# Kernel tuning notes

Measured on AMD Instinct MI355X. Metric: run time of the kernel, lower is better.

## Reference

```python
import jax, jax.numpy as jnp
import numpy as np

CONV_NUM = 8
CONV_SIZE = 96
HIDDEN = 768  # = CONV_NUM * CONV_SIZE
MAX_LEN = 128


def get_entity(x, s, e):
    # x: [B, L, H]; mean of x[i, s[i]:max(e[i], s[i]+1)] per sample (ragged gather+mean)
    e = jnp.maximum(e, s + 1)
    pos = jnp.arange(x.shape[1])  # [L]
    mask = (pos[None, :] >= s[:, None]) & (pos[None, :] < e[:, None])  # [B, L]
    m = mask.astype(x.dtype)
    return jnp.einsum('blh,bl->bh', x, m) / jnp.sum(m, axis=1, keepdims=True)


def feature_abstract(head_ent, tail_ent, x, fc_W, fc_b):
    # head_ent/tail_ent: [B, HIDDEN] -> per-sample conv filters; x: [B, HIDDEN]
    B = x.shape[0]
    wh = head_ent.reshape(B * CONV_NUM, 1, 1, CONV_SIZE)
    wt = tail_ent.reshape(B * CONV_NUM, 1, 1, CONV_SIZE)
    lhs = x.reshape(1, B, 1, HIDDEN)  # NCHW, groups=B -> per-sample correlation
    h = jax.nn.relu(jax.lax.conv_general_dilated(lhs, wh, (1, 1), 'VALID', feature_group_count=B))
    t = jax.nn.relu(jax.lax.conv_general_dilated(lhs, wt, (1, 1), 'VALID', feature_group_count=B))
    # h,t: [1, B*CONV_NUM, 1, T] with T = HIDDEN - CONV_SIZE + 1
    ht = jnp.concatenate([h, t], axis=3).reshape(B * CONV_NUM, -1)  # [B*cn, 2T]
    ht = ht.reshape(B * CONV_NUM, -1, 2).mean(axis=-1)  # AvgPool1d(k=2, s=2) -> [B*cn, T]
    flat = ht.reshape(B, -1)  # [B, cn*T] (dropout is identity in eval)
    return flat @ fc_W.T + fc_b  # [B, HIDDEN]


def setup_inputs() -> dict:
    key = jax.random.key(0)
    ks = jax.random.split(key, 16)
    Bs, Bq, L, H = 400, 1200, MAX_LEN, HIDDEN

    def spans(k1, k2, B):
        s = jax.random.randint(k1, (B,), 0, 100)
        e = jnp.minimum(s + jax.random.randint(k2, (B,), 1, 20), L)
        return s.astype(jnp.int64), e.astype(jnp.int64)

    s_eh, s_eh_end = spans(ks[0], ks[1], Bs)
    s_et, s_et_end = spans(ks[2], ks[3], Bs)
    q_eh, q_eh_end = spans(ks[4], ks[5], Bq)
    q_et, q_et_end = spans(ks[6], ks[7], Bq)
    fc_in = (H - CONV_SIZE + 1) * CONV_NUM  # 5384
    return {
        'all_support': jax.random.normal(ks[8], (Bs, L, H), jnp.float32),
        'support_emb': jax.random.normal(ks[9], (Bs, H), jnp.float32),
        'all_query': jax.random.normal(ks[10], (Bq, L, H), jnp.float32),
        'query_emb': jax.random.normal(ks[11], (Bq, H), jnp.float32),
        'fc_W': jax.random.normal(ks[12], (H, fc_in), jnp.float32) / np.sqrt(fc_in),
        'fc_b': jnp.zeros((H,), jnp.float32),
        's_eh': s_eh, 's_eh_end': s_eh_end, 's_et': s_et, 's_et_end': s_et_end,
        'q_eh': q_eh, 'q_eh_end': q_eh_end, 'q_et': q_et, 'q_et_end': q_et_end,
        'N': 10, 'K': 5, 'total_Q': 150,
    }


def reference(all_support, support_emb, all_query, query_emb, fc_W, fc_b,
              s_eh, s_eh_end, s_et, s_et_end, q_eh, q_eh_end, q_et, q_et_end,
              N, K, total_Q):
    sh = get_entity(all_support, s_eh, s_eh_end)
    st = get_entity(all_support, s_et, s_et_end)
    qh = get_entity(all_query, q_eh, q_eh_end)
    qt = get_entity(all_query, q_et, q_et_end)

    sup = feature_abstract(sh, st, support_emb, fc_W, fc_b).reshape(-1, N, K, HIDDEN)
    qry = feature_abstract(qh, qt, query_emb, fc_W, fc_b).reshape(-1, total_Q, HIDDEN)

    proto = sup.mean(axis=2)  # [Be, N, H]
    # -||proto - query||^2 over feature dim -> [Be, total_Q, N]
    diff = proto[:, None, :, :] - qry[:, :, None, :]
    logits = -jnp.sum(diff * diff, axis=-1)
    minn = logits.min(axis=-1)
    logits = jnp.concatenate([logits, minn[..., None] - 1.0], axis=2)  # [Be, total_Q, N+1]
    pred = jnp.argmax(logits.reshape(-1, N + 1), axis=1)
    return logits, pred
```

## Files before the change

kernel.cpp:

```cpp
#include <hip/hip_runtime.h>

#define H        768
#define LMAX     128
#define CONV_NUM 8
#define CONV_SIZE 96
#define T_CONV   673
#define FC_IN    5384
#define KP       5408
#define KSTEPS   (KP / 32)
#define N_WAY    10
#define K_SHOT   5
#define TOTAL_Q  150
#define SPLITK   8
#define BS       400
#define BQ       1200
#define MTOT     1600
#define NPROTO   80
#define MA       1280

using s16x8 = __attribute__((ext_vector_type(8))) short;
using f32x4 = __attribute__((ext_vector_type(4))) float;
typedef unsigned short u16;

__device__ __forceinline__ u16 f2bf(float x) {
    unsigned u = __float_as_uint(x);
    u += 0x7FFFu + ((u >> 16) & 1u);
    return (u16)(u >> 16);
}
__device__ __forceinline__ float bf2f(u16 b) { return __uint_as_float(((unsigned)b) << 16); }

__device__ __forceinline__ void gl16(const u16* g, u16* l) {
    __builtin_amdgcn_global_load_lds(
        (const __attribute__((address_space(1))) unsigned int*)g,
        (__attribute__((address_space(3))) unsigned int*)l, 16, 0, 0);
}

#define HTS 678
#define XCS 784
__global__ __launch_bounds__(256, 4) void pre_kernel(
    const float* __restrict__ all_support, const float* __restrict__ all_query,
    const float* __restrict__ support_emb, const float* __restrict__ query_emb,
    const float* __restrict__ fc_W,
    const int* __restrict__ s_eh, const int* __restrict__ s_eh_end,
    const int* __restrict__ s_et, const int* __restrict__ s_et_end,
    const int* __restrict__ q_eh, const int* __restrict__ q_eh_end,
    const int* __restrict__ q_et, const int* __restrict__ q_et_end,
    u16* __restrict__ flatS, u16* __restrict__ A_bf,
    u16* __restrict__ Wh)
{
    int bid = blockIdx.x;
    int tid = threadIdx.x;

    if (bid >= MTOT) {
        int r = bid - MTOT;
        const float* wr = fc_W + (size_t)r * FC_IN;
        u16* whr = Wh + (size_t)r * KP;
        for (int j4 = tid; j4 < KP / 4; j4 += 256) {
            int j = j4 * 4;
            ushort4 o;
            if (j4 < FC_IN / 4) {
                float4 v = *(const float4*)(wr + j);
                o.x = f2bf(v.x); o.y = f2bf(v.y); o.z = f2bf(v.z); o.w = f2bf(v.w);
            } else {
                o.x = 0; o.y = 0; o.z = 0; o.w = 0;
            }
            *(ushort4*)(whr + j) = o;
        }
        return;
    }

    __shared__ u16 htb[16 * HTS];
    __shared__ u16 filt_h[16 * 96];
    __shared__ u16 filt_l[16 * 96];
    __shared__ u16 xcs[8][XCS];

    int b = bid;
    const float* src;
    int sh, eh, st, et;
    if (b < BS) {
        src = all_support + (size_t)b * LMAX * H;
        sh = s_eh[b]; eh = s_eh_end[b]; st = s_et[b]; et = s_et_end[b];
    } else {
        int m = b - BS;
        src = all_query + (size_t)m * LMAX * H;
        sh = q_eh[m]; eh = q_eh_end[m]; st = q_et[m]; et = q_et_end[m];
    }
    if (eh < sh + 1) eh = sh + 1;
    if (et < st + 1) et = st + 1;

    {
        float a0 = 0.f, a1 = 0.f, a2 = 0.f, b0 = 0.f, b1 = 0.f, b2 = 0.f;
        float c0 = 0.f, c1 = 0.f, c2 = 0.f, d0 = 0.f, d1 = 0.f, d2 = 0.f;
        int r = sh;
        for (; r + 4 <= eh; r += 4) {
            const float* p0 = src + (size_t)r * H;
            const float* p1 = p0 + H;
            const float* p2 = p0 + 2 * H;
            const float* p3 = p0 + 3 * H;
            a0 += p0[tid]; a1 += p0[tid + 256]; a2 += p0[tid + 512];
            b0 += p1[tid]; b1 += p1[tid + 256]; b2 += p1[tid + 512];
            c0 += p2[tid]; c1 += p2[tid + 256]; c2 += p2[tid + 512];
            d0 += p3[tid]; d1 += p3[tid + 256]; d2 += p3[tid + 512];
        }
        for (; r < eh; ++r) {
            const float* p0 = src + (size_t)r * H;
            a0 += p0[tid]; a1 += p0[tid + 256]; a2 += p0[tid + 512];
        }
        float rc = 1.0f / (float)(eh - sh);
        float m0 = ((a0 + b0) + (c0 + d0)) * rc;
        float m1 = ((a1 + b1) + (c1 + d1)) * rc;
        float m2 = ((a2 + b2) + (c2 + d2)) * rc;
        u16 h0 = f2bf(m0), h1 = f2bf(m1), h2 = f2bf(m2);
        filt_h[tid] = h0;       filt_l[tid] = f2bf(m0 - bf2f(h0));
        filt_h[tid + 256] = h1; filt_l[tid + 256] = f2bf(m1 - bf2f(h1));
        filt_h[tid + 512] = h2; filt_l[tid + 512] = f2bf(m2 - bf2f(h2));
        a0 = a1 = a2 = b0 = b1 = b2 = c0 = c1 = c2 = d0 = d1 = d2 = 0.f;
        r = st;
        for (; r + 4 <= et; r += 4) {
            const float* p0 = src + (size_t)r * H;
            const float* p1 = p0 + H;
            const float* p2 = p0 + 2 * H;
            const float* p3 = p0 + 3 * H;
            a0 += p0[tid]; a1 += p0[tid + 256]; a2 += p0[tid + 512];
            b0 += p1[tid]; b1 += p1[tid + 256]; b2 += p1[tid + 512];
            c0 += p2[tid]; c1 += p2[tid + 256]; c2 += p2[tid + 512];
            d0 += p3[tid]; d1 += p3[tid + 256]; d2 += p3[tid + 512];
        }
        for (; r < et; ++r) {
            const float* p0 = src + (size_t)r * H;
            a0 += p0[tid]; a1 += p0[tid + 256]; a2 += p0[tid + 512];
        }
        rc = 1.0f / (float)(et - st);
        m0 = ((a0 + b0) + (c0 + d0)) * rc;
        m1 = ((a1 + b1) + (c1 + d1)) * rc;
        m2 = ((a2 + b2) + (c2 + d2)) * rc;
        h0 = f2bf(m0); h1 = f2bf(m1); h2 = f2bf(m2);
        filt_h[tid + 768] = h0;  filt_l[tid + 768] = f2bf(m0 - bf2f(h0));
        filt_h[tid + 1024] = h1; filt_l[tid + 1024] = f2bf(m1 - bf2f(h1));
        filt_h[tid + 1280] = h2; filt_l[tid + 1280] = f2bf(m2 - bf2f(h2));
    }

    {
        if (tid < 192) {
            int row = tid / 24, idx = tid % 24;
            int j = 768 - row + idx;
            if (j < XCS) xcs[row][j] = 0;
        }
        if (tid >= 192 && tid < 192 + 80) {
            int t = tid - 192;
            htb[(t / 5) * HTS + 673 + (t % 5)] = 0;
        }
        const float* xsrc = (b < BS) ? (support_emb + (size_t)b * H)
                                     : (query_emb + (size_t)(b - BS) * H);
        if (tid < 192) {
            float4 v = *(const float4*)(xsrc + tid * 4);
            u16 h[4] = {f2bf(v.x), f2bf(v.y), f2bf(v.z), f2bf(v.w)};
            #pragma unroll
            for (int u = 0; u < 4; ++u) {
                int i = tid * 4 + u;
                #pragma unroll
                for (int c = 0; c < 8; ++c)
                    if (i >= c) xcs[c][i - c] = h[u];
            }
        }
    }
    __syncthreads();

    {
        int lane = tid & 63, wv = tid >> 6;
        int n = lane & 15, g = lane >> 4;
        int afo = n * 96 + g * 8;
        s16x8 fh0 = *(const s16x8*)&filt_h[afo];
        s16x8 fh1 = *(const s16x8*)&filt_h[afo + 32];
        s16x8 fh2 = *(const s16x8*)&filt_h[afo + 64];
        s16x8 fl0 = *(const s16x8*)&filt_l[afo];
        s16x8 fl1 = *(const s16x8*)&filt_l[afo + 32];
        s16x8 fl2 = *(const s16x8*)&filt_l[afo + 64];
        const u16* xrow = &xcs[n & 7][g * 8 + (n & 8)];
        #pragma unroll 1
        for (int nt = wv; nt < 43; nt += 4) {
            const u16* xp = xrow + nt * 16;
            s16x8 x0 = *(const s16x8*)(xp);
            s16x8 x1 = *(const s16x8*)(xp + 32);
            s16x8 x2 = *(const s16x8*)(xp + 64);
            f32x4 a = (f32x4){0.f, 0.f, 0.f, 0.f};
            a = __builtin_amdgcn_mfma_f32_16x16x32_bf16(fh0, x0, a, 0, 0, 0);
            a = __builtin_amdgcn_mfma_f32_16x16x32_bf16(fl0, x0, a, 0, 0, 0);
            a = __builtin_amdgcn_mfma_f32_16x16x32_bf16(fh1, x1, a, 0, 0, 0);
            a = __builtin_amdgcn_mfma_f32_16x16x32_bf16(fl1, x1, a, 0, 0, 0);
            a = __builtin_amdgcn_mfma_f32_16x16x32_bf16(fh2, x2, a, 0, 0, 0);
            a = __builtin_amdgcn_mfma_f32_16x16x32_bf16(fl2, x2, a, 0, 0, 0);
            int pcol = nt * 16 + n;
            if (pcol < T_CONV) {
                #pragma unroll
                for (int r = 0; r < 4; ++r)
                    htb[(g * 4 + r) * HTS + pcol] = f2bf(fmaxf(a[r], 0.f));
            }
        }
    }
    __syncthreads();

    u16* oh = (b < BS) ? (flatS + (size_t)b * KP)
                       : (A_bf + (size_t)(NPROTO + b - BS) * KP);
    for (int t = tid; t < KP / 8; t += 256) {
        int i0 = t * 8;
        s16x8 o;
        if (i0 < FC_IN) {
            #pragma unroll
            for (int u = 0; u < 8; ++u) {
                int i = i0 + u;
                int f = (int)(((unsigned)i * 24929u) >> 24);
                int j = i - f * 673;
                int e0 = 2 * j, e1 = 2 * j + 1;
                float v0 = bf2f((e0 < T_CONV) ? htb[f * HTS + e0]
                                              : htb[(8 + f) * HTS + (e0 - T_CONV)]);
                float v1 = bf2f((e1 < T_CONV) ? htb[f * HTS + e1]
                                              : htb[(8 + f) * HTS + (e1 - T_CONV)]);
                o[u] = (short)f2bf(0.5f * (v0 + v1));
            }
        } else {
            #pragma unroll
            for (int u = 0; u < 8; ++u) o[u] = 0;
        }
        *(s16x8*)(oh + i0) = o;
    }
}

__global__ __launch_bounds__(256) void avg_kernel(
    const u16* __restrict__ flatS, u16* __restrict__ A_bf)
{
    int i = blockIdx.x;
    int t = blockIdx.y * 256 + threadIdx.x;
    if (t >= KP / 8) return;
    size_t base = (size_t)i * K_SHOT * KP;
    int j = t * 8;
    float s[8] = {0.f, 0.f, 0.f, 0.f, 0.f, 0.f, 0.f, 0.f};
    #pragma unroll
    for (int k = 0; k < K_SHOT; ++k) {
        s16x8 vh = *(const s16x8*)(flatS + base + (size_t)k * KP + j);
        #pragma unroll
        for (int u = 0; u < 8; ++u)
            s[u] += bf2f((u16)vh[u]);
    }
    s16x8 oh;
    #pragma unroll
    for (int u = 0; u < 8; ++u)
        oh[u] = (short)f2bf(s[u] * (1.0f / K_SHOT));
    *(s16x8*)(A_bf + (size_t)i * KP + j) = oh;
}

#define ASEG 4096
#define BSEG 4096
#define BUFU (ASEG + BSEG)

#define STAGE(ks, buf) do {                                     \
    int kb_ = (ks) * 32;                                        \
    u16* L_ = &lds[buf][0];                                     \
    gl16(Ah_g + aoff0 + kb_, L_ + cA0 * 8);                     \
    gl16(Ah_g + aoff1 + kb_, L_ + cA1 * 8);                     \
    gl16(Bh_g + boff0 + kb_, L_ + ASEG + cA0 * 8);              \
    gl16(Bh_g + boff1 + kb_, L_ + ASEG + cA1 * 8);              \
} while (0)

__global__ __launch_bounds__(256, 3) void gemm_mfma(
    const u16* __restrict__ Ah_g, const u16* __restrict__ Bh_g,
    u16* __restrict__ partsB)
{
    __shared__ u16 lds[2][BUFU];

    int tid = threadIdx.x;
    int wg = (blockIdx.x & 7) * 60 + (blockIdx.x >> 3);
    int sk = wg / 60;
    int rem = wg % 60;
    int n0 = (rem / 10) * 128;
    int m0 = (rem % 10) * 128;

    int ks0 = (KSTEPS * sk) / SPLITK;
    int nk = (KSTEPS * (sk + 1)) / SPLITK - ks0;

    int cA0 = tid, cA1 = tid + 256;
    size_t aoff0 = (size_t)(m0 + (cA0 >> 6) * 16 + (cA0 & 15)) * KP + ((cA0 >> 4) & 3) * 8;
    size_t aoff1 = (size_t)(m0 + (cA1 >> 6) * 16 + (cA1 & 15)) * KP + ((cA1 >> 4) & 3) * 8;
    size_t boff0 = (size_t)(n0 + (cA0 >> 6) * 16 + (cA0 & 15)) * KP + ((cA0 >> 4) & 3) * 8;
    size_t boff1 = (size_t)(n0 + (cA1 >> 6) * 16 + (cA1 & 15)) * KP + ((cA1 >> 4) & 3) * 8;

    int w = tid >> 6, lane = tid & 63;
    int wm = w >> 1, wn = w & 1;
    int lfr = ((lane >> 4) * 16 + (lane & 15)) * 8;

    f32x4 acc[4][4];
    #pragma unroll
    for (int i = 0; i < 4; ++i)
        #pragma unroll
        for (int j = 0; j < 4; ++j) acc[i][j] = (f32x4){0.f, 0.f, 0.f, 0.f};

    STAGE(ks0, 0);
    STAGE(ks0 + 1, 1);

    int cur = 0;
    for (int k = 0; k < nk; ++k) {
        if (k + 1 < nk) asm volatile("s_waitcnt vmcnt(4)" ::: "memory");
        else            asm volatile("s_waitcnt vmcnt(0)" ::: "memory");
        __builtin_amdgcn_s_barrier();

        const u16* L = &lds[cur][0];
        s16x8 ah[4], bh[4];
        #pragma unroll
        for (int f = 0; f < 4; ++f) {
            ah[f] = *(const s16x8*)(L + (wm * 4 + f) * 512 + lfr);
            bh[f] = *(const s16x8*)(L + ASEG + (wn * 4 + f) * 512 + lfr);
        }
        asm volatile("s_waitcnt lgkmcnt(0)" ::: "memory");
        __builtin_amdgcn_s_barrier();

        if (k + 2 < nk) STAGE(ks0 + k + 2, cur);

        #pragma unroll
        for (int i = 0; i < 4; ++i)
            #pragma unroll
            for (int j = 0; j < 4; ++j)
                acc[i][j] = __builtin_amdgcn_mfma_f32_16x16x32_bf16(ah[i], bh[j], acc[i][j], 0, 0, 0);
        cur ^= 1;
    }

    int rbase = m0 + wm * 64 + (lane >> 4) * 4;
    int cbase = n0 + wn * 64 + (lane & 15);
    #pragma unroll
    for (int i = 0; i < 4; ++i) {
        int row0 = rbase + i * 16;
        #pragma unroll
        for (int j = 0; j < 4; ++j) {
            int col = cbase + j * 16;
            u16* dst = partsB + ((size_t)sk * MA + row0) * H + col;
            #pragma unroll
            for (int r = 0; r < 4; ++r)
                dst[(size_t)r * H] = f2bf(acc[i][j][r]);
        }
    }
}

__global__ __launch_bounds__(192) void protofin_kernel(
    const u16* __restrict__ partsB, float* __restrict__ proto)
{
    int i = blockIdx.x;
    int d0 = threadIdx.x * 4;
    float s0 = 0.f, s1 = 0.f, s2 = 0.f, s3 = 0.f;
    #pragma unroll
    for (int sp = 0; sp < SPLITK; ++sp) {
        ushort4 v = *(const ushort4*)(partsB + ((size_t)sp * MA + i) * H + d0);
        s0 += bf2f(v.x); s1 += bf2f(v.y); s2 += bf2f(v.z); s3 += bf2f(v.w);
    }
    *(float4*)(proto + (size_t)i * H + d0) = make_float4(s0, s1, s2, s3);
}

__global__ __launch_bounds__(192) void dist_kernel(
    const u16* __restrict__ partsB, const float* __restrict__ proto,
    float* __restrict__ outp)
{
    int bid = blockIdx.x;
    int e = bid / TOTAL_Q;
    int tid = threadIdx.x;
    int m = NPROTO + bid;
    int d0 = tid * 4;

    float qv0 = 0.f, qv1 = 0.f, qv2 = 0.f, qv3 = 0.f;
    #pragma unroll
    for (int sp = 0; sp < SPLITK; ++sp) {
        ushort4 v = *(const ushort4*)(partsB + ((size_t)sp * MA + m) * H + d0);
        qv0 += bf2f(v.x); qv1 += bf2f(v.y); qv2 += bf2f(v.z); qv3 += bf2f(v.w);
    }

    __shared__ float red[N_WAY][3];
    __shared__ float lvals[N_WAY];
    int wave = tid >> 6, lane = tid & 63;
    for (int n = 0; n < N_WAY; ++n) {
        const float* pr = proto + (size_t)(e * N_WAY + n) * H + d0;
        float4 pv = *(const float4*)pr;
        float df0 = pv.x - qv0, df1 = pv.y - qv1, df2 = pv.z - qv2, df3 = pv.w - qv3;
        float p = df0 * df0;
        p = fmaf(df1, df1, p);
        p = fmaf(df2, df2, p);
        p = fmaf(df3, df3, p);
        #pragma unroll
        for (int off = 32; off > 0; off >>= 1)
            p += __shfl_down(p, off);
        if (lane == 0) red[n][wave] = p;
    }
    __syncthreads();
    if (tid < N_WAY) {
        float v = red[tid][0] + red[tid][1] + red[tid][2];
        lvals[tid] = -v;
        outp[(size_t)bid * (N_WAY + 1) + tid] = -v;
    }
    __syncthreads();
    if (tid == 0) {
        float mn = lvals[0];
        #pragma unroll
        for (int n = 1; n < N_WAY; ++n) mn = fminf(mn, lvals[n]);
        float last = mn - 1.0f;
        outp[(size_t)bid * (N_WAY + 1) + N_WAY] = last;
        float best = lvals[0];
        int bi = 0;
        for (int n = 1; n < N_WAY; ++n)
            if (lvals[n] > best) { best = lvals[n]; bi = n; }
        if (last > best) bi = N_WAY;
        outp[(size_t)BQ * (N_WAY + 1) + bid] = (float)bi;
    }
}

extern "C" void kernel_launch(void* const* d_in, const int* in_sizes, int n_in,
                              void* d_out, int out_size, void* d_ws, size_t ws_size,
                              hipStream_t stream)
{
    const float* all_support = (const float*)d_in[0];
    const float* support_emb = (const float*)d_in[1];
    const float* all_query   = (const float*)d_in[2];
    const float* query_emb   = (const float*)d_in[3];
    const float* fc_W        = (const float*)d_in[4];
    const int* s_eh     = (const int*)d_in[6];
    const int* s_eh_end = (const int*)d_in[7];
    const int* s_et     = (const int*)d_in[8];
    const int* s_et_end = (const int*)d_in[9];
    const int* q_eh     = (const int*)d_in[10];
    const int* q_eh_end = (const int*)d_in[11];
    const int* q_et     = (const int*)d_in[12];
    const int* q_et_end = (const int*)d_in[13];

    u16* partsB  = (u16*)d_ws;
    float* proto = (float*)(partsB + (size_t)SPLITK * MA * H);
    u16* Wh      = (u16*)(proto + (size_t)NPROTO * H);
    u16* A_bf    = Wh + (size_t)H * KP;
    u16* flatS   = A_bf + (size_t)MA * KP;

    pre_kernel<<<MTOT + H, 256, 0, stream>>>(
        all_support, all_query, support_emb, query_emb, fc_W,
        s_eh, s_eh_end, s_et, s_et_end, q_eh, q_eh_end, q_et, q_et_end,
        flatS, A_bf, Wh);

    avg_kernel<<<dim3(NPROTO, 3), 256, 0, stream>>>(flatS, A_bf);

    gemm_mfma<<<480, 256, 0, stream>>>(A_bf, Wh, partsB);

    protofin_kernel<<<NPROTO, 192, 0, stream>>>(partsB, proto);

    dist_kernel<<<BQ, 192, 0, stream>>>(partsB, proto, (float*)d_out);
}
```

Measured before the change: 68.74 us.

## Drop support averaging kernel; run all 1600 rows through GEMM and average after

Removes the avg_kernel that averaged the K support flattened features before the FC GEMM. All 400 support rows now go through the GEMM directly, and the prototype mean is taken in protofin over the GEMM outputs, which is valid because the FC layer is linear. This saves a launch and one intermediate buffer round trip, but the GEMM grows from 1280 to 1600 rows (624 blocks instead of 480) and needs row clamping. The span-mean gather is also rewritten to use float4 loads across 192 threads.

```diff
diff --git a/kernel.cpp b/kernel.cpp
--- a/kernel.cpp
+++ b/kernel.cpp
@@ -16,7 +16,6 @@
 #define BQ       1200
 #define MTOT     1600
 #define NPROTO   80
-#define MA       1280
 
 using s16x8 = __attribute__((ext_vector_type(8))) short;
 using f32x4 = __attribute__((ext_vector_type(4))) float;
@@ -45,8 +44,7 @@
     const int* __restrict__ s_et, const int* __restrict__ s_et_end,
     const int* __restrict__ q_eh, const int* __restrict__ q_eh_end,
     const int* __restrict__ q_et, const int* __restrict__ q_et_end,
-    u16* __restrict__ flatS, u16* __restrict__ A_bf,
-    u16* __restrict__ Wh)
+    u16* __restrict__ A_bf, u16* __restrict__ Wh)
 {
     int bid = blockIdx.x;
     int tid = threadIdx.x;
@@ -88,56 +86,38 @@
     if (eh < sh + 1) eh = sh + 1;
     if (et < st + 1) et = st + 1;
 
-    {
-        float a0 = 0.f, a1 = 0.f, a2 = 0.f, b0 = 0.f, b1 = 0.f, b2 = 0.f;
-        float c0 = 0.f, c1 = 0.f, c2 = 0.f, d0 = 0.f, d1 = 0.f, d2 = 0.f;
-        int r = sh;
-        for (; r + 4 <= eh; r += 4) {
-            const float* p0 = src + (size_t)r * H;
-            const float* p1 = p0 + H;
-            const float* p2 = p0 + 2 * H;
-            const float* p3 = p0 + 3 * H;
-            a0 += p0[tid]; a1 += p0[tid + 256]; a2 += p0[tid + 512];
-            b0 += p1[tid]; b1 += p1[tid + 256]; b2 += p1[tid + 512];
-            c0 += p2[tid]; c1 += p2[tid + 256]; c2 += p2[tid + 512];
-            d0 += p3[tid]; d1 += p3[tid + 256]; d2 += p3[tid + 512];
-        }
-        for (; r < eh; ++r) {
-            const float* p0 = src + (size_t)r * H;
-            a0 += p0[tid]; a1 += p0[tid + 256]; a2 += p0[tid + 512];
-        }
-        float rc = 1.0f / (float)(eh - sh);
-        float m0 = ((a0 + b0) + (c0 + d0)) * rc;
-        float m1 = ((a1 + b1) + (c1 + d1)) * rc;
-        float m2 = ((a2 + b2) + (c2 + d2)) * rc;
-        u16 h0 = f2bf(m0), h1 = f2bf(m1), h2 = f2bf(m2);
-        filt_h[tid] = h0;       filt_l[tid] = f2bf(m0 - bf2f(h0));
-        filt_h[tid + 256] = h1; filt_l[tid + 256] = f2bf(m1 - bf2f(h1));
-        filt_h[tid + 512] = h2; filt_l[tid + 512] = f2bf(m2 - bf2f(h2));
-        a0 = a1 = a2 = b0 = b1 = b2 = c0 = c1 = c2 = d0 = d1 = d2 = 0.f;
-        r = st;
-        for (; r + 4 <= et; r += 4) {
-            const float* p0 = src + (size_t)r * H;
-            const float* p1 = p0 + H;
-            const float* p2 = p0 + 2 * H;
-            const float* p3 = p0 + 3 * H;
-            a0 += p0[tid]; a1 += p0[tid + 256]; a2 += p0[tid + 512];
-            b0 += p1[tid]; b1 += p1[tid + 256]; b2 += p1[tid + 512];
-            c0 += p2[tid]; c1 += p2[tid + 256]; c2 += p2[tid + 512];
-            d0 += p3[tid]; d1 += p3[tid + 256]; d2 += p3[tid + 512];
-        }
-        for (; r < et; ++r) {
-            const float* p0 = src + (size_t)r * H;
-            a0 += p0[tid]; a1 += p0[tid + 256]; a2 += p0[tid + 512];
-        }
-        rc = 1.0f / (float)(et - st);
-        m0 = ((a0 + b0) + (c0 + d0)) * rc;
-        m1 = ((a1 + b1) + (c1 + d1)) * rc;
-        m2 = ((a2 + b2) + (c2 + d2)) * rc;
-        h0 = f2bf(m0); h1 = f2bf(m1); h2 = f2bf(m2);
-        filt_h[tid + 768] = h0;  filt_l[tid + 768] = f2bf(m0 - bf2f(h0));
-        filt_h[tid + 1024] = h1; filt_l[tid + 1024] = f2bf(m1 - bf2f(h1));
-        filt_h[tid + 1280] = h2; filt_l[tid + 1280] = f2bf(m2 - bf2f(h2));
+    if (tid < 192) {
+        const float4* base4 = (const float4*)src;
+        #pragma unroll 1
+        for (int ent = 0; ent < 2; ++ent) {
+            int rs = ent ? st : sh, re = ent ? et : eh;
+            float4 va = {0.f,0.f,0.f,0.f}, vb = va, vc = va, vd = va;
+            int r = rs;
+            for (; r + 4 <= re; r += 4) {
+                const float4* p = base4 + (size_t)r * 192 + tid;
+                float4 v0 = p[0], v1 = p[192], v2 = p[384], v3 = p[576];
+                va.x += v0.x; va.y += v0.y; va.z += v0.z; va.w += v0.w;
+                vb.x += v1.x; vb.y += v1.y; vb.z += v1.z; vb.w += v1.w;
+                vc.x += v2.x; vc.y += v2.y; vc.z += v2.z; vc.w += v2.w;
+                vd.x += v3.x; vd.y += v3.y; vd.z += v3.z; vd.w += v3.w;
+            }
+            for (; r < re; ++r) {
+                float4 v0 = base4[(size_t)r * 192 + tid];
+                va.x += v0.x; va.y += v0.y; va.z += v0.z; va.w += v0.w;
+            }
+            float rc = 1.0f / (float)(re - rs);
+            float mm[4] = {((va.x + vb.x) + (vc.x + vd.x)) * rc,
+                           ((va.y + vb.y) + (vc.y + vd.y)) * rc,
+                           ((va.z + vb.z) + (vc.z + vd.z)) * rc,
+                           ((va.w + vb.w) + (vc.w + vd.w)) * rc};
+            int o = ent * 768 + tid * 4;
+            #pragma unroll
+            for (int u = 0; u < 4; ++u) {
+                u16 hb = f2bf(mm[u]);
+                filt_h[o + u] = hb;
+                filt_l[o + u] = f2bf(mm[u] - bf2f(hb));
+            }
+        }
     }
 
     {
@@ -200,8 +180,7 @@
     }
     __syncthreads();
 
-    u16* oh = (b < BS) ? (flatS + (size_t)b * KP)
-                       : (A_bf + (size_t)(NPROTO + b - BS) * KP);
+    u16* oh = A_bf + (size_t)b * KP;
     for (int t = tid; t < KP / 8; t += 256) {
         int i0 = t * 8;
         s16x8 o;
@@ -226,32 +205,8 @@
     }
 }
 
-__global__ __launch_bounds__(256) void avg_kernel(
-    const u16* __restrict__ flatS, u16* __restrict__ A_bf)
-{
-    int i = blockIdx.x;
-    int t = blockIdx.y * 256 + threadIdx.x;
-    if (t >= KP / 8) return;
-    size_t base = (size_t)i * K_SHOT * KP;
-    int j = t * 8;
-    float s[8] = {0.f, 0.f, 0.f, 0.f, 0.f, 0.f, 0.f, 0.f};
-    #pragma unroll
-    for (int k = 0; k < K_SHOT; ++k) {
-        s16x8 vh = *(const s16x8*)(flatS + base + (size_t)k * KP + j);
-        #pragma unroll
-        for (int u = 0; u < 8; ++u)
-            s[u] += bf2f((u16)vh[u]);
-    }
-    s16x8 oh;
-    #pragma unroll
-    for (int u = 0; u < 8; ++u)
-        oh[u] = (short)f2bf(s[u] * (1.0f / K_SHOT));
-    *(s16x8*)(A_bf + (size_t)i * KP + j) = oh;
-}
-
 #define ASEG 4096
-#define BSEG 4096
-#define BUFU (ASEG + BSEG)
+#define BUFU (2 * ASEG)
 
 #define STAGE(ks, buf) do {                                     \
     int kb_ = (ks) * 32;                                        \
@@ -269,18 +224,20 @@
     __shared__ u16 lds[2][BUFU];
 
     int tid = threadIdx.x;
-    int wg = (blockIdx.x & 7) * 60 + (blockIdx.x >> 3);
-    int sk = wg / 60;
-    int rem = wg % 60;
-    int n0 = (rem / 10) * 128;
-    int m0 = (rem % 10) * 128;
+    int wg = (blockIdx.x & 7) * 78 + (blockIdx.x >> 3);
+    int sk = wg / 78;
+    int rem = wg % 78;
+    int n0 = (rem / 13) * 128;
+    int m0 = (rem % 13) * 128;
 
     int ks0 = (KSTEPS * sk) / SPLITK;
     int nk = (KSTEPS * (sk + 1)) / SPLITK - ks0;
 
     int cA0 = tid, cA1 = tid + 256;
-    size_t aoff0 = (size_t)(m0 + (cA0 >> 6) * 16 + (cA0 & 15)) * KP + ((cA0 >> 4) & 3) * 8;
-    size_t aoff1 = (size_t)(m0 + (cA1 >> 6) * 16 + (cA1 & 15)) * KP + ((cA1 >> 4) & 3) * 8;
+    int ar0 = m0 + (cA0 >> 6) * 16 + (cA0 & 15); if (ar0 >= MTOT) ar0 = MTOT - 1;
+    int ar1 = m0 + (cA1 >> 6) * 16 + (cA1 & 15); if (ar1 >= MTOT) ar1 = MTOT - 1;
+    size_t aoff0 = (size_t)ar0 * KP + ((cA0 >> 4) & 3) * 8;
+    size_t aoff1 = (size_t)ar1 * KP + ((cA1 >> 4) & 3) * 8;
     size_t boff0 = (size_t)(n0 + (cA0 >> 6) * 16 + (cA0 & 15)) * KP + ((cA0 >> 4) & 3) * 8;
     size_t boff1 = (size_t)(n0 + (cA1 >> 6) * 16 + (cA1 & 15)) * KP + ((cA1 >> 4) & 3) * 8;
 
@@ -331,10 +288,10 @@
         #pragma unroll
         for (int j = 0; j < 4; ++j) {
             int col = cbase + j * 16;
-            u16* dst = partsB + ((size_t)sk * MA + row0) * H + col;
+            u16* dst = partsB + ((size_t)sk * MTOT + row0) * H + col;
             #pragma unroll
             for (int r = 0; r < 4; ++r)
-                dst[(size_t)r * H] = f2bf(acc[i][j][r]);
+                if (row0 + r < MTOT) dst[(size_t)r * H] = f2bf(acc[i][j][r]);
         }
     }
 }
@@ -342,15 +299,21 @@
 __global__ __launch_bounds__(192) void protofin_kernel(
     const u16* __restrict__ partsB, float* __restrict__ proto)
 {
-    int i = blockIdx.x;
+    int g = blockIdx.x;
     int d0 = threadIdx.x * 4;
     float s0 = 0.f, s1 = 0.f, s2 = 0.f, s3 = 0.f;
     #pragma unroll
     for (int sp = 0; sp < SPLITK; ++sp) {
-        ushort4 v = *(const ushort4*)(partsB + ((size_t)sp * MA + i) * H + d0);
-        s0 += bf2f(v.x); s1 += bf2f(v.y); s2 += bf2f(v.z); s3 += bf2f(v.w);
-    }
-    *(float4*)(proto + (size_t)i * H + d0) = make_float4(s0, s1, s2, s3);
+        #pragma unroll
+        for (int k = 0; k < K_SHOT; ++k) {
+            size_t row = (size_t)sp * MTOT + g * K_SHOT + k;
+            ushort4 v = *(const ushort4*)(partsB + row * H + d0);
+            s0 += bf2f(v.x); s1 += bf2f(v.y); s2 += bf2f(v.z); s3 += bf2f(v.w);
+        }
+    }
+    float sc = 1.0f / K_SHOT;
+    *(float4*)(proto + (size_t)g * H + d0) =
+        make_float4(s0 * sc, s1 * sc, s2 * sc, s3 * sc);
 }
 
 __global__ __launch_bounds__(192) void dist_kernel(
@@ -360,13 +323,13 @@
     int bid = blockIdx.x;
     int e = bid / TOTAL_Q;
     int tid = threadIdx.x;
-    int m = NPROTO + bid;
+    int m = BS + bid;
     int d0 = tid * 4;
 
     float qv0 = 0.f, qv1 = 0.f, qv2 = 0.f, qv3 = 0.f;
     #pragma unroll
     for (int sp = 0; sp < SPLITK; ++sp) {
-        ushort4 v = *(const ushort4*)(partsB + ((size_t)sp * MA + m) * H + d0);
+        ushort4 v = *(const ushort4*)(partsB + ((size_t)sp * MTOT + m) * H + d0);
         qv0 += bf2f(v.x); qv1 += bf2f(v.y); qv2 += bf2f(v.z); qv3 += bf2f(v.w);
     }
 
@@ -427,19 +390,16 @@
     const int* q_et_end = (const int*)d_in[13];
 
     u16* partsB  = (u16*)d_ws;
-    float* proto = (float*)(partsB + (size_t)SPLITK * MA * H);
+    float* proto = (float*)(partsB + (size_t)SPLITK * MTOT * H);
     u16* Wh      = (u16*)(proto + (size_t)NPROTO * H);
     u16* A_bf    = Wh + (size_t)H * KP;
-    u16* flatS   = A_bf + (size_t)MA * KP;
 
     pre_kernel<<<MTOT + H, 256, 0, stream>>>(
         all_support, all_query, support_emb, query_emb, fc_W,
         s_eh, s_eh_end, s_et, s_et_end, q_eh, q_eh_end, q_et, q_et_end,
-        flatS, A_bf, Wh);
-
-    avg_kernel<<<dim3(NPROTO, 3), 256, 0, stream>>>(flatS, A_bf);
-
-    gemm_mfma<<<480, 256, 0, stream>>>(A_bf, Wh, partsB);
+        A_bf, Wh);
+
+    gemm_mfma<<<624, 256, 0, stream>>>(A_bf, Wh, partsB);
 
     protofin_kernel<<<NPROTO, 192, 0, stream>>>(partsB, proto);
 
```

New measurement: 75.63 us. 1.1x slower.
